# Optimization experiments

Measured on AMD Instinct MI355X. Metric: run time of the kernel, lower is better.

The kernel has to match this reference:

```python
import jax, jax.numpy as jnp
import numpy as np

# Module hyperparams (from init_kwargs)
MAX_DISP = 4
DILA = 1
P = 2 * MAX_DISP // DILA + 1  # patch_size = 9 -> 81 output channels


def setup_inputs() -> dict:
    key = jax.random.key(0)
    k0, k1 = jax.random.split(key)
    B, C, H, W = 4, 256, 96, 160
    return {
        "fmap0": jax.random.normal(k0, (B, C, H, W), dtype=jnp.float32),
        "fmap1": jax.random.normal(k1, (B, C, H, W), dtype=jnp.float32),
    }


def reference(fmap0, fmap1):
    """SpatialCorrelationSampler(kernel_size=1, patch_size=P, stride=1,
    padding=0, dilation=1, dilation_patch=DILA), reshaped to (B, P*P, H, W).

    corr[b, p, y, x] = sum_c fmap0[b,c,y,x] * fmap1[b,c,y+dy_p,x+dx_p]
    with (dy,dx) in {-MAX_DISP..MAX_DISP step DILA}; out-of-bounds -> 0
    (no channel normalization, matching the CUDA sampler).
    """
    B, C, H, W = fmap0.shape
    D = MAX_DISP
    # Zero-pad fmap1 so every displacement is a static-size slice.
    padded = jnp.pad(fmap1, ((0, 0), (0, 0), (D, D), (D, D)))
    oy, ox = jnp.meshgrid(jnp.arange(P) * DILA, jnp.arange(P) * DILA, indexing="ij")
    offs = jnp.stack([oy.ravel(), ox.ravel()], axis=1)  # (P*P, 2)

    def one_disp(off):
        # window of fmap1 shifted by (off - D): (B, C, H, W)
        win = jax.lax.dynamic_slice(padded, (0, 0, off[0], off[1]), (B, C, H, W))
        return jnp.einsum("bchw,bchw->bhw", fmap0, win)

    corr = jax.lax.map(one_disp, offs)  # (P*P, B, H, W), avoids P^2*C blowup
    return jnp.transpose(corr, (1, 0, 2, 3))  # (B, P*P, H, W)
```

## Files before the change

kernel.cpp:

```cpp
#include <hip/hip_runtime.h>


#define Bn 4
#define Cn 256
#define Hn 96
#define Wn 160
#define HWn (Hn * Wn)
#define NP 81
#define TY 16
#define TX 16
#define CCH 8
#define NSTAGE (Cn / CCH)
#define WROWS (TY + 8)
#define SEGS 6
#define LROW 28
#define F1C (WROWS * LROW)
#define BUF (CCH * F1C)
#define NT 576
#define F1STG (CCH * HWn / 4)

__global__ __launch_bounds__(NT, 2) void corr_kernel(const float* __restrict__ f0,
                                                     const float* __restrict__ f1,
                                                     float* __restrict__ out) {
    __shared__ __align__(16) float lds[2 * BUF];

    const int tid  = threadIdx.x;
    const int wave = tid >> 6;
    const int lane = tid & 63;
    const int r    = lane >> 2;
    const int g    = lane & 3;

    const int blk = blockIdx.x;
    const int xcd = blk & 7;
    const int it  = blk >> 3;
    const int b   = xcd >> 1;
    const int ty  = (xcd & 1) * 3 + it / 10;
    const int tx  = it % 10;
    const int y0  = ty * TY;
    const int x0  = tx * TX;

    const int scc  = tid / (WROWS * SEGS);
    const int srm  = tid - scc * (WROWS * SEGS);
    const int srr  = srm / SEGS;
    const int sseg = srm - srr * SEGS;
    const int sgy  = y0 - 4 + srr;
    const int sgx  = x0 - 4 + sseg * 4;
    const bool sval = (sgy >= 0) && (sgy < Hn) && (sgx >= 0) && (sgx < Wn);
    const int slidx = (scc * F1C + srr * LROW + sseg * 4) >> 2;
    const int sgidx = sval ? ((((b * Cn + scc) * Hn + sgy) * Wn + sgx) >> 2) : 0;

    const float4* __restrict__ f1v = (const float4*)f1;
    float4* lv = (float4*)lds;

    float4 p1a = make_float4(0.f, 0.f, 0.f, 0.f), p1b = p1a;
    if (sval) { p1a = f1v[sgidx]; p1b = f1v[sgidx + HWn]; }

    const float* f0s = f0 + ((b * Cn) * Hn + y0 + r) * Wn + x0 + g * 4;
    float4 p0[CCH];
#pragma unroll
    for (int cc = 0; cc < CCH; ++cc) p0[cc] = *(const float4*)(f0s + cc * HWn);

    float acc[9][4];
#pragma unroll
    for (int i = 0; i < 9; ++i)
#pragma unroll
        for (int j = 0; j < 4; ++j) acc[i][j] = 0.f;

    for (int s = 0; s < NSTAGE; ++s) {
        float4* buf = lv + (s & 1) * (BUF / 4);
        buf[slidx]       = p1a;
        buf[slidx + F1C] = p1b;
        __syncthreads();

        const int ns = (s + 1 < NSTAGE) ? s + 1 : NSTAGE - 1;
        float4 n1a = make_float4(0.f, 0.f, 0.f, 0.f), n1b = n1a;
        if (sval) { n1a = f1v[sgidx + ns * F1STG]; n1b = f1v[sgidx + ns * F1STG + HWn]; }
        float4 n0[CCH];
#pragma unroll
        for (int cc = 0; cc < CCH; ++cc)
            n0[cc] = *(const float4*)(f0s + (ns * CCH + cc) * HWn);

        const float* base = &lds[(s & 1) * BUF + (r + wave) * LROW + g * 4];
#pragma unroll
        for (int cc = 0; cc < CCH; ++cc) {
            const float* wr = base + cc * F1C;
            float4 w0 = *(const float4*)(wr);
            float4 w1 = *(const float4*)(wr + 4);
            float4 w2 = *(const float4*)(wr + 8);
            float av[4]  = {p0[cc].x, p0[cc].y, p0[cc].z, p0[cc].w};
            float wv[12] = {w0.x, w0.y, w0.z, w0.w, w1.x, w1.y, w1.z, w1.w,
                            w2.x, w2.y, w2.z, w2.w};
#pragma unroll
            for (int dx = 0; dx < 9; ++dx)
#pragma unroll
                for (int rx = 0; rx < 4; ++rx)
                    acc[dx][rx] = fmaf(av[rx], wv[rx + dx], acc[dx][rx]);
        }

        p1a = n1a; p1b = n1b;
#pragma unroll
        for (int cc = 0; cc < CCH; ++cc) p0[cc] = n0[cc];
    }

    const int orow = ((b * NP + wave * 9) * Hn + y0 + r) * Wn + x0 + g * 4;
#pragma unroll
    for (int dx = 0; dx < 9; ++dx)
        *(float4*)(out + orow + dx * HWn) =
            make_float4(acc[dx][0], acc[dx][1], acc[dx][2], acc[dx][3]);
}

extern "C" void kernel_launch(void* const* d_in, const int* in_sizes, int n_in,
                              void* d_out, int out_size, void* d_ws, size_t ws_size,
                              hipStream_t stream) {
    const float* f0 = (const float*)d_in[0];
    const float* f1 = (const float*)d_in[1];
    float* out = (float*)d_out;
    corr_kernel<<<dim3(240), NT, 0, stream>>>(f0, f1, out);
}
```

Before: 183.0 us.

## Stage fmap0 through LDS via direct global-to-LDS loads and swizzle fmap1 rows

Each f0 chunk is now loaded once per block into double-buffered LDS with global_load_lds, issued by eight waves. Previously all nine waves loaded the same f0 values into registers, so this removes the redundant global/L2 traffic and frees about 64 VGPRs of prefetch registers. The fmap1 LDS row stride is padded from 28 to 32 floats, and reads and writes use an XOR swizzle on alternate rows to reduce bank conflicts. The cost is extra LDS use and extra LDS reads for f0 in the inner loop. Correctness relies on the asynchronous LDS loads having completed before the next barrier.

```diff
diff --git a/kernel.cpp b/kernel.cpp
--- a/kernel.cpp
+++ b/kernel.cpp
@@ -13,16 +13,19 @@
 #define NSTAGE (Cn / CCH)
 #define WROWS (TY + 8)
 #define SEGS 6
-#define LROW 28
+#define LROW 32
 #define F1C (WROWS * LROW)
-#define BUF (CCH * F1C)
+#define F1BUF (CCH * F1C)
+#define F0C (TY * TX)
+#define F0BUF (CCH * F0C)
 #define NT 576
 #define F1STG (CCH * HWn / 4)
 
 __global__ __launch_bounds__(NT, 2) void corr_kernel(const float* __restrict__ f0,
                                                      const float* __restrict__ f1,
                                                      float* __restrict__ out) {
-    __shared__ __align__(16) float lds[2 * BUF];
+    __shared__ __align__(16) float f1lds[2 * F1BUF];
+    __shared__ __align__(16) float f0lds[2 * F0BUF];
 
     const int tid  = threadIdx.x;
     const int wave = tid >> 6;
@@ -46,19 +49,29 @@
     const int sgy  = y0 - 4 + srr;
     const int sgx  = x0 - 4 + sseg * 4;
     const bool sval = (sgy >= 0) && (sgy < Hn) && (sgx >= 0) && (sgx < Wn);
-    const int slidx = (scc * F1C + srr * LROW + sseg * 4) >> 2;
+    const int swz   = (sseg * 4) ^ ((srr & 1) << 4);
+    const int slidx = (scc * F1C + srr * LROW + swz) >> 2;
     const int sgidx = sval ? ((((b * Cn + scc) * Hn + sgy) * Wn + sgx) >> 2) : 0;
 
     const float4* __restrict__ f1v = (const float4*)f1;
-    float4* lv = (float4*)lds;
+    float4* f1lv = (float4*)f1lds;
 
+    const int q  = r + wave;
+    const int xr = (q & 1) << 4;
+    const int o0 = q * LROW + ((g * 4) ^ xr);
+    const int o1 = q * LROW + ((g * 4 + 4) ^ xr);
+    const int o2 = q * LROW + ((g * 4 + 8) ^ xr);
+
+    const float* f0g0 = f0 + ((b * Cn + wave) * Hn + y0 + (lane >> 2)) * Wn
+                      + x0 + (lane & 3) * 4;
+
+    if (wave < 8) {
+        __builtin_amdgcn_global_load_lds(
+            (const __attribute__((address_space(1))) void*)f0g0,
+            (__attribute__((address_space(3))) void*)&f0lds[wave * F0C], 16, 0, 0);
+    }
     float4 p1a = make_float4(0.f, 0.f, 0.f, 0.f), p1b = p1a;
     if (sval) { p1a = f1v[sgidx]; p1b = f1v[sgidx + HWn]; }
-
-    const float* f0s = f0 + ((b * Cn) * Hn + y0 + r) * Wn + x0 + g * 4;
-    float4 p0[CCH];
-#pragma unroll
-    for (int cc = 0; cc < CCH; ++cc) p0[cc] = *(const float4*)(f0s + cc * HWn);
 
     float acc[9][4];
 #pragma unroll
@@ -67,27 +80,32 @@
         for (int j = 0; j < 4; ++j) acc[i][j] = 0.f;
 
     for (int s = 0; s < NSTAGE; ++s) {
-        float4* buf = lv + (s & 1) * (BUF / 4);
+        float4* buf = f1lv + (s & 1) * (F1BUF / 4);
         buf[slidx]       = p1a;
         buf[slidx + F1C] = p1b;
         __syncthreads();
 
-        const int ns = (s + 1 < NSTAGE) ? s + 1 : NSTAGE - 1;
-        float4 n1a = make_float4(0.f, 0.f, 0.f, 0.f), n1b = n1a;
-        if (sval) { n1a = f1v[sgidx + ns * F1STG]; n1b = f1v[sgidx + ns * F1STG + HWn]; }
-        float4 n0[CCH];
-#pragma unroll
-        for (int cc = 0; cc < CCH; ++cc)
-            n0[cc] = *(const float4*)(f0s + (ns * CCH + cc) * HWn);
+        const int ns = s + 1;
+        if (ns < NSTAGE) {
+            if (wave < 8) {
+                __builtin_amdgcn_global_load_lds(
+                    (const __attribute__((address_space(1))) void*)(f0g0 + ns * (CCH * HWn)),
+                    (__attribute__((address_space(3))) void*)&f0lds[(ns & 1) * F0BUF + wave * F0C],
+                    16, 0, 0);
+            }
+            if (sval) { p1a = f1v[sgidx + ns * F1STG]; p1b = f1v[sgidx + ns * F1STG + HWn]; }
+        }
 
-        const float* base = &lds[(s & 1) * BUF + (r + wave) * LROW + g * 4];
+        const float* fb  = &f1lds[(s & 1) * F1BUF];
+        const float* f0b = &f0lds[(s & 1) * F0BUF + (r << 4) + (g << 2)];
 #pragma unroll
         for (int cc = 0; cc < CCH; ++cc) {
-            const float* wr = base + cc * F1C;
-            float4 w0 = *(const float4*)(wr);
-            float4 w1 = *(const float4*)(wr + 4);
-            float4 w2 = *(const float4*)(wr + 8);
-            float av[4]  = {p0[cc].x, p0[cc].y, p0[cc].z, p0[cc].w};
+            const float* wr = fb + cc * F1C;
+            float4 w0 = *(const float4*)(wr + o0);
+            float4 w1 = *(const float4*)(wr + o1);
+            float4 w2 = *(const float4*)(wr + o2);
+            float4 a4 = *(const float4*)(f0b + cc * F0C);
+            float av[4]  = {a4.x, a4.y, a4.z, a4.w};
             float wv[12] = {w0.x, w0.y, w0.z, w0.w, w1.x, w1.y, w1.z, w1.w,
                             w2.x, w2.y, w2.z, w2.w};
 #pragma unroll
@@ -96,10 +114,6 @@
                 for (int rx = 0; rx < 4; ++rx)
                     acc[dx][rx] = fmaf(av[rx], wv[rx + dx], acc[dx][rx]);
         }
-
-        p1a = n1a; p1b = n1b;
-#pragma unroll
-        for (int cc = 0; cc < CCH; ++cc) p0[cc] = n0[cc];
     }
 
     const int orow = ((b * NP + wave * 9) * Hn + y0 + r) * Wn + x0 + g * 4;
```

After: 185.2 us. No clear change (+1.2%).

## Split channel reduction across two blocks with ticket-based reduction and swizzled LDS

Applied to the files above, without the earlier changes.

Splits the 256-channel reduction into two halves, doubling the grid from 240 to 480 blocks. Each block writes its partial sums to a workspace, and the last block to finish a tile (found through an atomic ticket) adds the other half and writes the output. When no workspace is available it falls back to atomic adds into a zeroed output. It also widens the LDS row stride and XOR-swizzles it to cut bank conflicts. The cost is extra partial-buffer traffic, a memset launch and fence/atomic synchronization, in exchange for better occupancy of the 256 CUs.

```diff
diff --git a/kernel.cpp b/kernel.cpp
--- a/kernel.cpp
+++ b/kernel.cpp
@@ -3,6 +3,7 @@
 
 #define Bn 4
 #define Cn 256
+#define CHALF 128
 #define Hn 96
 #define Wn 160
 #define HWn (Hn * Wn)
@@ -10,19 +11,25 @@
 #define TY 16
 #define TX 16
 #define CCH 8
-#define NSTAGE (Cn / CCH)
+#define NSTAGE (CHALF / CCH)
 #define WROWS (TY + 8)
 #define SEGS 6
-#define LROW 28
+#define LROW 32
 #define F1C (WROWS * LROW)
 #define BUF (CCH * F1C)
 #define NT 576
 #define F1STG (CCH * HWn / 4)
+#define NPART (Bn * NP * Hn * Wn)
+#define WS_NEED ((size_t)NPART * 8 + 4096)
 
 __global__ __launch_bounds__(NT, 2) void corr_kernel(const float* __restrict__ f0,
                                                      const float* __restrict__ f1,
-                                                     float* __restrict__ out) {
+                                                     float* __restrict__ out,
+                                                     float* __restrict__ pbuf,
+                                                     int* __restrict__ tickets,
+                                                     int use_ws) {
     __shared__ __align__(16) float lds[2 * BUF];
+    __shared__ int who;
 
     const int tid  = threadIdx.x;
     const int wave = tid >> 6;
@@ -30,14 +37,18 @@
     const int r    = lane >> 2;
     const int g    = lane & 3;
 
-    const int blk = blockIdx.x;
-    const int xcd = blk & 7;
-    const int it  = blk >> 3;
-    const int b   = xcd >> 1;
-    const int ty  = (xcd & 1) * 3 + it / 10;
-    const int tx  = it % 10;
-    const int y0  = ty * TY;
-    const int x0  = tx * TX;
+    const int blk  = blockIdx.x;
+    const int xcd  = blk & 7;
+    const int it2  = blk >> 3;
+    const int half = it2 / 30;
+    const int it   = it2 % 30;
+    const int b    = xcd >> 1;
+    const int ty   = (xcd & 1) * 3 + it / 10;
+    const int tx   = it % 10;
+    const int y0   = ty * TY;
+    const int x0   = tx * TX;
+    const int ch0  = half * CHALF;
+    const int tile_id = xcd * 30 + it;
 
     const int scc  = tid / (WROWS * SEGS);
     const int srm  = tid - scc * (WROWS * SEGS);
@@ -46,16 +57,23 @@
     const int sgy  = y0 - 4 + srr;
     const int sgx  = x0 - 4 + sseg * 4;
     const bool sval = (sgy >= 0) && (sgy < Hn) && (sgx >= 0) && (sgx < Wn);
-    const int slidx = (scc * F1C + srr * LROW + sseg * 4) >> 2;
-    const int sgidx = sval ? ((((b * Cn + scc) * Hn + sgy) * Wn + sgx) >> 2) : 0;
+    const int swz   = (sseg * 4) ^ ((srr & 1) << 4);
+    const int slidx = (scc * F1C + srr * LROW + swz) >> 2;
+    const int sgidx = sval ? ((((b * Cn + ch0 + scc) * Hn + sgy) * Wn + sgx) >> 2) : 0;
 
     const float4* __restrict__ f1v = (const float4*)f1;
     float4* lv = (float4*)lds;
 
+    const int q  = r + wave;
+    const int xr = (q & 1) << 4;
+    const int o0 = q * LROW + ((g * 4) ^ xr);
+    const int o1 = q * LROW + ((g * 4 + 4) ^ xr);
+    const int o2 = q * LROW + ((g * 4 + 8) ^ xr);
+
     float4 p1a = make_float4(0.f, 0.f, 0.f, 0.f), p1b = p1a;
     if (sval) { p1a = f1v[sgidx]; p1b = f1v[sgidx + HWn]; }
 
-    const float* f0s = f0 + ((b * Cn) * Hn + y0 + r) * Wn + x0 + g * 4;
+    const float* f0s = f0 + ((b * Cn + ch0) * Hn + y0 + r) * Wn + x0 + g * 4;
     float4 p0[CCH];
 #pragma unroll
     for (int cc = 0; cc < CCH; ++cc) p0[cc] = *(const float4*)(f0s + cc * HWn);
@@ -80,13 +98,13 @@
         for (int cc = 0; cc < CCH; ++cc)
             n0[cc] = *(const float4*)(f0s + (ns * CCH + cc) * HWn);
 
-        const float* base = &lds[(s & 1) * BUF + (r + wave) * LROW + g * 4];
+        const float* base = &lds[(s & 1) * BUF];
 #pragma unroll
         for (int cc = 0; cc < CCH; ++cc) {
             const float* wr = base + cc * F1C;
-            float4 w0 = *(const float4*)(wr);
-            float4 w1 = *(const float4*)(wr + 4);
-            float4 w2 = *(const float4*)(wr + 8);
+            float4 w0 = *(const float4*)(wr + o0);
+            float4 w1 = *(const float4*)(wr + o1);
+            float4 w2 = *(const float4*)(wr + o2);
             float av[4]  = {p0[cc].x, p0[cc].y, p0[cc].z, p0[cc].w};
             float wv[12] = {w0.x, w0.y, w0.z, w0.w, w1.x, w1.y, w1.z, w1.w,
                             w2.x, w2.y, w2.z, w2.w};
@@ -103,10 +121,34 @@
     }
 
     const int orow = ((b * NP + wave * 9) * Hn + y0 + r) * Wn + x0 + g * 4;
+    if (use_ws) {
+        float* pmine = pbuf + (size_t)half * NPART;
 #pragma unroll
-    for (int dx = 0; dx < 9; ++dx)
-        *(float4*)(out + orow + dx * HWn) =
-            make_float4(acc[dx][0], acc[dx][1], acc[dx][2], acc[dx][3]);
+        for (int dx = 0; dx < 9; ++dx)
+            *(float4*)(pmine + orow + dx * HWn) =
+                make_float4(acc[dx][0], acc[dx][1], acc[dx][2], acc[dx][3]);
+        __threadfence();
+        __syncthreads();
+        if (tid == 0) who = atomicAdd(&tickets[tile_id], 1);
+        __syncthreads();
+        if (who == 1) {
+            __threadfence();
+            const float* pother = pbuf + (size_t)(1 - half) * NPART;
+#pragma unroll
+            for (int dx = 0; dx < 9; ++dx) {
+                float4 o = *(const float4*)(pother + orow + dx * HWn);
+                *(float4*)(out + orow + dx * HWn) =
+                    make_float4(acc[dx][0] + o.x, acc[dx][1] + o.y,
+                                acc[dx][2] + o.z, acc[dx][3] + o.w);
+            }
+        }
+    } else {
+#pragma unroll
+        for (int dx = 0; dx < 9; ++dx)
+#pragma unroll
+            for (int rx = 0; rx < 4; ++rx)
+                atomicAdd(out + orow + dx * HWn + rx, acc[dx][rx]);
+    }
 }
 
 extern "C" void kernel_launch(void* const* d_in, const int* in_sizes, int n_in,
@@ -115,5 +157,13 @@
     const float* f0 = (const float*)d_in[0];
     const float* f1 = (const float*)d_in[1];
     float* out = (float*)d_out;
-    corr_kernel<<<dim3(240), NT, 0, stream>>>(f0, f1, out);
+    int use_ws = (d_ws != nullptr && ws_size >= WS_NEED) ? 1 : 0;
+    float* pbuf = (float*)d_ws;
+    int* tickets = (int*)((char*)d_ws + (size_t)NPART * 8);
+    if (use_ws) {
+        hipMemsetAsync(tickets, 0, 240 * sizeof(int), stream);
+    } else {
+        hipMemsetAsync(d_out, 0, out_size, stream);
+    }
+    corr_kernel<<<dim3(480), NT, 0, stream>>>(f0, f1, out, pbuf, tickets, use_ws);
 }
```

After: 404.0 us. 2.21x slower.
